# Optimization experiments

Hardware: AMD Instinct MI355X
Metric: run time of the kernel (lower is better)

## Reference

```python
import jax, jax.numpy as jnp
import numpy as np

B, C, D = 512, 100000, 512
MARGIN = 0.5  # ArcFace-style additive angular margin


def setup_inputs() -> dict:
    key = jax.random.key(0)
    k1, k2, k3 = jax.random.split(key, 3)
    embeddings = jax.random.normal(k1, (B, D), dtype=jnp.float32)
    labels = jax.random.randint(k2, (B,), 0, C, dtype=jnp.int32)
    weight = 0.01 * jax.random.normal(k3, (C, D), dtype=jnp.float32)  # torch.normal(0, 0.01, (C, D))
    return {"embeddings": embeddings, "labels": labels, "weight": weight}


def _l2_normalize(x, eps=1e-12):
    return x / jnp.maximum(jnp.linalg.norm(x, axis=-1, keepdims=True), eps)


def reference(embeddings, labels, weight):
    cos_m = jnp.cos(MARGIN)
    sin_m = jnp.sin(MARGIN)

    e = _l2_normalize(embeddings)          # (B, D)
    w = _l2_normalize(weight)              # (C, D)
    logits = jnp.clip(jnp.einsum('bd,cd->bc', e, w), -1.0, 1.0)  # (B, C) cosines

    bsz, ncls = logits.shape
    rows = jnp.arange(bsz)
    cos_t = logits[rows, labels]                                   # (B,) cos(theta_y)
    sin_t = jnp.sqrt(jnp.clip(1.0 - cos_t * cos_t, 0.0, None))     # sin(theta_y)
    cos_tm = cos_t * cos_m - sin_t * sin_m                         # cos(theta_y + m)
    sin_tm = sin_t * cos_m + cos_t * sin_m                         # sin(theta_y + m)

    # non-target class indices per row, ascending, skipping the target: (B, C-1)
    base = jnp.arange(ncls - 1)[None, :]
    nt_idx = base + (base >= labels[:, None]).astype(base.dtype)

    # margin_softmax: logits2 = cos(theta_j) - cos(theta_y + m) over non-target j
    nt_logits = jnp.take_along_axis(logits, nt_idx, axis=1)       # (B, C-1)
    logits2 = nt_logits - cos_tm[:, None]

    # no_grad block: weight_m is unit-norm point at angle theta_y+m from e,
    # so ||w_j - w_m||^2 = 2 - 2 <w_j, w_m>  (avoids materializing (B, C, D)).
    w_y = w[labels]                                                # (B, D)
    w_m = (-sin_m * e + sin_tm[:, None] * w_y) / sin_t[:, None]    # (B, D), unit norm
    sim = jnp.einsum('bd,cd->bc', w_m, w)                          # (B, C)
    nt_sim = jnp.take_along_axis(sim, nt_idx, axis=1)              # (B, C-1)
    diff_weight_norm = jax.lax.stop_gradient(
        jnp.sqrt(jnp.clip(2.0 - 2.0 * nt_sim, 0.0, None)))         # (B, C-1)

    e_logits = jnp.sum(jnp.exp(logits2 / diff_weight_norm), axis=1)  # (B,)
    return jnp.mean(jnp.log1p(e_logits))
```

## Files before the change

### kernel.cpp

```cpp
#include <hip/hip_runtime.h>
#include <hip/hip_fp8.h>
#include <math.h>

#define B_SZ 512
#define C_SZ 100000
#define D_SZ 512

#define BM 128
#define BN 128
#define BK 64
#define NTILES 782
#define MT 8
#define NBLK (NTILES * MT)
#define KSTEPS 8
#define DEPTH 2

typedef __attribute__((ext_vector_type(4))) float f32x4;
typedef __attribute__((ext_vector_type(16))) float f32x16;
typedef __attribute__((ext_vector_type(4))) int i32x4;
typedef __attribute__((ext_vector_type(8))) int i32x8;

#define UNITY_SCALE 0x7F7F7F7F

__device__ __forceinline__ void gload_lds16(const void* gptr, void* lptr) {
  __builtin_amdgcn_global_load_lds(
      (const __attribute__((address_space(1))) void*)gptr,
      (__attribute__((address_space(3))) void*)lptr,
      16, 0, 0);
}

__device__ __forceinline__ unsigned char f2fp8(float x) {
  __hip_fp8_e4m3 h(x);
  return (unsigned char)h.__x;
}
__device__ __forceinline__ float fp82f(unsigned int u) {
  __hip_fp8_e4m3 h;
  h.__x = (unsigned char)u;
  return (float)h;
}
__device__ __forceinline__ unsigned int pack4f8(float a, float b, float c, float d) {
  return (unsigned int)f2fp8(a) | ((unsigned int)f2fp8(b) << 8) |
         ((unsigned int)f2fp8(c) << 16) | ((unsigned int)f2fp8(d) << 24);
}

__device__ __forceinline__ i32x8 ld_frag(const unsigned char* base, int frag, int l) {
  i32x4 lo = *(const i32x4*)(base + frag * 2048 + l * 16);
  i32x4 hg = *(const i32x4*)(base + frag * 2048 + 1024 + l * 16);
  return __builtin_shufflevector(lo, hg, 0, 1, 2, 3, 4, 5, 6, 7);
}

__global__ __launch_bounds__(256) void k_norm_w(const float* __restrict__ w,
                                                unsigned char* __restrict__ w8) {
  const int row = blockIdx.x * 4 + (threadIdx.x >> 6);
  const int lane = threadIdx.x & 63;
  const float4* wr = (const float4*)(w + (size_t)row * D_SZ);
  float4 v0 = wr[lane];
  float4 v1 = wr[64 + lane];
  float ss = v0.x*v0.x + v0.y*v0.y + v0.z*v0.z + v0.w*v0.w
           + v1.x*v1.x + v1.y*v1.y + v1.z*v1.z + v1.w*v1.w;
  #pragma unroll
  for (int o = 32; o; o >>= 1) ss += __shfl_xor(ss, o, 64);
  const float rn = __builtin_amdgcn_rsqf(fmaxf(ss, 1e-24f));
  unsigned int* out = (unsigned int*)(w8 + (size_t)row * D_SZ);
  out[lane] = pack4f8(v0.x * rn, v0.y * rn, v0.z * rn, v0.w * rn);
  out[64 + lane] = pack4f8(v1.x * rn, v1.y * rn, v1.z * rn, v1.w * rn);
}

__global__ __launch_bounds__(64) void k_prep(const float* __restrict__ e,
                                             const int* __restrict__ labels,
                                             const unsigned char* __restrict__ w8,
                                             unsigned char* __restrict__ A8,
                                             float4* __restrict__ params) {
  const int b = blockIdx.x;
  const int lane = threadIdx.x;
  const float4* er = (const float4*)(e + (size_t)b * D_SZ);
  float4 v0 = er[lane], v1 = er[64 + lane];
  float ss = v0.x*v0.x + v0.y*v0.y + v0.z*v0.z + v0.w*v0.w
           + v1.x*v1.x + v1.y*v1.y + v1.z*v1.z + v1.w*v1.w;
  #pragma unroll
  for (int o = 32; o; o >>= 1) ss += __shfl_xor(ss, o, 64);
  const float rn = __builtin_amdgcn_rsqf(fmaxf(ss, 1e-24f));
  v0.x *= rn; v0.y *= rn; v0.z *= rn; v0.w *= rn;
  v1.x *= rn; v1.y *= rn; v1.z *= rn; v1.w *= rn;

  unsigned int* arow_e = (unsigned int*)(A8 + (size_t)(2 * b) * D_SZ);
  arow_e[lane] = pack4f8(v0.x, v0.y, v0.z, v0.w);
  arow_e[64 + lane] = pack4f8(v1.x, v1.y, v1.z, v1.w);

  const int lab = labels[b];
  const unsigned int* wr = (const unsigned int*)(w8 + (size_t)lab * D_SZ);
  unsigned int w0 = wr[lane], w1 = wr[64 + lane];
  unsigned int* arow_w = (unsigned int*)(A8 + (size_t)(2 * b + 1) * D_SZ);
  arow_w[lane] = w0;
  arow_w[64 + lane] = w1;

  float d = v0.x * fp82f(w0 & 255) + v0.y * fp82f((w0 >> 8) & 255)
          + v0.z * fp82f((w0 >> 16) & 255) + v0.w * fp82f(w0 >> 24)
          + v1.x * fp82f(w1 & 255) + v1.y * fp82f((w1 >> 8) & 255)
          + v1.z * fp82f((w1 >> 16) & 255) + v1.w * fp82f(w1 >> 24);
  #pragma unroll
  for (int o = 32; o; o >>= 1) d += __shfl_xor(d, o, 64);

  if (lane == 0) {
    const float cos_m = 0.877582561890372716f;
    const float sin_m = 0.479425538604203000f;
    float cos_t = fminf(fmaxf(d, -1.0f), 1.0f);
    float sin_t = sqrtf(fmaxf(1.0f - cos_t * cos_t, 0.0f));
    float cos_tm = cos_t * cos_m - sin_t * sin_m;
    float sin_tm = sin_t * cos_m + cos_t * sin_m;
    float inv_st = 1.0f / fmaxf(sin_t, 1e-20f);
    params[b] = make_float4(cos_tm, sin_m * inv_st, sin_tm * inv_st, 0.0f);
  }
}

__device__ __forceinline__ float termf(float de, float dwy, float4 p, bool kill) {
  float c = fminf(fmaxf(de, -1.0f), 1.0f);
  float s = p.z * dwy - p.y * de;
  float x = fmaxf(fmaf(-2.0f, s, 2.0f), 1e-20f);
  float t = (c - p.x) * __builtin_amdgcn_rsqf(x);
  float r = __expf(t);
  return kill ? 0.0f : r;
}

__global__ __launch_bounds__(512, 8) void k_gemm(const unsigned char* __restrict__ A8,
                                                 const unsigned char* __restrict__ W8,
                                                 const float4* __restrict__ params,
                                                 const int* __restrict__ labels,
                                                 float* __restrict__ part) {
  __shared__ __align__(32) unsigned char At[DEPTH][BM * BK];
  __shared__ __align__(32) unsigned char Bt[DEPTH][BN * BK];
  __shared__ float ered[64];
  __shared__ float4 pl[64];
  __shared__ int ll[64];

  const int bid = blockIdx.x;
  const int p = (bid & 7) * (NBLK / 8) + (bid >> 3);
  const int nt = p >> 3, mt = p & 7;
  const int t = threadIdx.x;
  const int w = t >> 6, l = t & 63;
  const int m0 = mt * BM;
  const int n0 = nt * BN;
  const int b0 = mt * 64;

  if (t < 64) {
    ered[t] = 0.0f;
    pl[t] = params[b0 + t];
    ll[t] = labels[b0 + t];
  }

  const int kpart = ((t >> 5) & 1) * 32 + ((t >> 6) & 1) * 16;
  const int aoffs = (m0 + (t >> 7) * 32 + (t & 31)) * D_SZ + kpart;
  int brow_s = n0 + (t >> 7) * 32 + (t & 31);
  if (brow_s >= C_SZ) brow_s = C_SZ - 1;
  const int boffs = brow_s * D_SZ + kpart;

  f32x16 accA = {}, accB = {};
  const int fA = w & 3;
  const int fB0 = (w >> 2) * 2;
  const int hi = l >> 5;

#define STAGE(d, ts)                                                        \
  do {                                                                      \
    const int k0_ = (ts) * BK;                                              \
    gload_lds16(A8 + aoffs + k0_, (void*)(At[d] + t * 16));                 \
    gload_lds16(W8 + (size_t)(boffs + k0_), (void*)(Bt[d] + t * 16));       \
  } while (0)

  STAGE(0, 0);
  STAGE(1, 1);
  asm volatile("s_waitcnt vmcnt(2) lgkmcnt(0)" ::: "memory");
  __builtin_amdgcn_s_barrier();

  #pragma unroll
  for (int s = 0; s < KSTEPS; ++s) {
    const int d = s & 1;
    i32x8 av = ld_frag(At[d], fA, l);
    i32x8 bv = ld_frag(Bt[d], fB0, l);
    __builtin_amdgcn_s_setprio(1);
    accA = __builtin_amdgcn_mfma_scale_f32_32x32x64_f8f6f4(
        av, bv, accA, 0, 0, 0, UNITY_SCALE, 0, UNITY_SCALE);
    bv = ld_frag(Bt[d], fB0 + 1, l);
    accB = __builtin_amdgcn_mfma_scale_f32_32x32x64_f8f6f4(
        av, bv, accB, 0, 0, 0, UNITY_SCALE, 0, UNITY_SCALE);
    __builtin_amdgcn_s_setprio(0);
    if (s < KSTEPS - 1) {
      asm volatile("s_waitcnt vmcnt(0)" ::: "memory");
      __builtin_amdgcn_s_barrier();
      if (s + 2 < KSTEPS)
        STAGE(d, s + 2);
    }
  }
#undef STAGE

  #pragma unroll
  for (int rp = 0; rp < 8; ++rp) {
    const int r = 2 * rp;
    const int lb = fA * 16 + (rp & 1) + 4 * (rp >> 1) + 2 * hi;
    float4 pp = pl[lb];
    int lab = ll[lb];
    int j0 = n0 + fB0 * 32 + (l & 31);
    int j1 = j0 + 32;
    float s = termf(accA[r], accA[r + 1], pp, (j0 >= C_SZ) || (j0 == lab))
            + termf(accB[r], accB[r + 1], pp, (j1 >= C_SZ) || (j1 == lab));
    #pragma unroll
    for (int o = 1; o < 32; o <<= 1) s += __shfl_xor(s, o, 64);
    if ((l & 31) == 0) atomicAdd(&ered[lb], s);
  }
  __syncthreads();
  if (t < 64) part[(size_t)(b0 + t) * NTILES + nt] = ered[t];
}

__global__ __launch_bounds__(256) void k_rowsum(const float* __restrict__ part,
                                                float* __restrict__ rowsum) {
  const int b = blockIdx.x;
  float s = 0.0f;
  for (int i = threadIdx.x; i < NTILES; i += 256) s += part[(size_t)b * NTILES + i];
  #pragma unroll
  for (int o = 32; o; o >>= 1) s += __shfl_xor(s, o, 64);
  __shared__ float red[4];
  if ((threadIdx.x & 63) == 0) red[threadIdx.x >> 6] = s;
  __syncthreads();
  if (threadIdx.x == 0)
    rowsum[b] = log1pf(red[0] + red[1] + red[2] + red[3]);
}

__global__ __launch_bounds__(512) void k_final(const float* __restrict__ rowsum,
                                               float* __restrict__ out) {
  const int b = threadIdx.x;
  float v = rowsum[b];
  __shared__ float red[512];
  red[b] = v;
  __syncthreads();
  #pragma unroll
  for (int o = 256; o; o >>= 1) {
    if (b < o) red[b] += red[b + o];
    __syncthreads();
  }
  if (b == 0) out[0] = red[0] / (float)B_SZ;
}

extern "C" void kernel_launch(void* const* d_in, const int* in_sizes, int n_in,
                              void* d_out, int out_size, void* d_ws, size_t ws_size,
                              hipStream_t stream) {
  const float* emb = (const float*)d_in[0];
  const int* labels = (const int*)d_in[1];
  const float* w = (const float*)d_in[2];

  char* ws = (char*)d_ws;
  unsigned char* w8 = (unsigned char*)ws;
  size_t off = (size_t)C_SZ * D_SZ;
  unsigned char* A8 = (unsigned char*)(ws + off);
  off += (size_t)2 * B_SZ * D_SZ;
  float4* params = (float4*)(ws + off);
  off += (size_t)B_SZ * 16;
  float* part = (float*)(ws + off);
  off += (size_t)B_SZ * NTILES * 4;
  float* rowsum = (float*)(ws + off);
  off += (size_t)B_SZ * 4;

  k_norm_w<<<dim3(C_SZ / 4), dim3(256), 0, stream>>>(w, w8);
  k_prep<<<dim3(B_SZ), dim3(64), 0, stream>>>(emb, labels, w8, A8, params);
  k_gemm<<<dim3(NBLK), dim3(512), 0, stream>>>(A8, w8, params, labels, part);
  k_rowsum<<<dim3(B_SZ), dim3(256), 0, stream>>>(part, rowsum);
  k_final<<<dim3(1), dim3(512), 0, stream>>>(rowsum, (float*)d_out);
}
```

Measured before the change: 146.6 us.

## Double GEMM block M-tile to 256 with 2x2 MFMA accumulators per wave

Raises the block M tile from 128 to 256 rows, so each wave computes a 2x2 grid of 32x32 MFMA outputs instead of 1x2, and halves the number of blocks along M. Each loaded W tile is reused across twice as many rows, cutting global and LDS traffic per MFMA. In exchange it uses more LDS and accumulator registers per block, lowers the occupancy hint from 8 to 4, and spreads the epilogue over more rows per block.

```diff
diff --git a/kernel.cpp b/kernel.cpp
--- a/kernel.cpp
+++ b/kernel.cpp
@@ -6,11 +6,11 @@
 #define C_SZ 100000
 #define D_SZ 512
 
-#define BM 128
+#define BM 256
 #define BN 128
 #define BK 64
 #define NTILES 782
-#define MT 8
+#define MT 4
 #define NBLK (NTILES * MT)
 #define KSTEPS 8
 #define DEPTH 2
@@ -122,66 +122,75 @@
   return kill ? 0.0f : r;
 }
 
-__global__ __launch_bounds__(512, 8) void k_gemm(const unsigned char* __restrict__ A8,
+__global__ __launch_bounds__(512, 4) void k_gemm(const unsigned char* __restrict__ A8,
                                                  const unsigned char* __restrict__ W8,
                                                  const float4* __restrict__ params,
                                                  const int* __restrict__ labels,
                                                  float* __restrict__ part) {
   __shared__ __align__(32) unsigned char At[DEPTH][BM * BK];
   __shared__ __align__(32) unsigned char Bt[DEPTH][BN * BK];
-  __shared__ float ered[64];
-  __shared__ float4 pl[64];
-  __shared__ int ll[64];
+  __shared__ float ered[128];
+  __shared__ float4 pl[128];
+  __shared__ int ll[128];
 
   const int bid = blockIdx.x;
   const int p = (bid & 7) * (NBLK / 8) + (bid >> 3);
-  const int nt = p >> 3, mt = p & 7;
+  const int nt = p >> 2, mt = p & 3;
   const int t = threadIdx.x;
   const int w = t >> 6, l = t & 63;
   const int m0 = mt * BM;
   const int n0 = nt * BN;
-  const int b0 = mt * 64;
-
-  if (t < 64) {
+  const int b0 = mt * 128;
+
+  if (t < 128) {
     ered[t] = 0.0f;
     pl[t] = params[b0 + t];
     ll[t] = labels[b0 + t];
   }
 
   const int kpart = ((t >> 5) & 1) * 32 + ((t >> 6) & 1) * 16;
-  const int aoffs = (m0 + (t >> 7) * 32 + (t & 31)) * D_SZ + kpart;
+  const int aoffs0 = (m0 + (t >> 7) * 32 + (t & 31)) * D_SZ + kpart;
+  const int aoffs1 = aoffs0 + 128 * D_SZ;
   int brow_s = n0 + (t >> 7) * 32 + (t & 31);
   if (brow_s >= C_SZ) brow_s = C_SZ - 1;
   const int boffs = brow_s * D_SZ + kpart;
 
-  f32x16 accA = {}, accB = {};
-  const int fA = w & 3;
+  f32x16 acc00 = {}, acc01 = {}, acc10 = {}, acc11 = {};
+  const int fA0 = (w & 3) * 2;
   const int fB0 = (w >> 2) * 2;
   const int hi = l >> 5;
 
 #define STAGE(d, ts)                                                        \
   do {                                                                      \
     const int k0_ = (ts) * BK;                                              \
-    gload_lds16(A8 + aoffs + k0_, (void*)(At[d] + t * 16));                 \
+    gload_lds16(A8 + aoffs0 + k0_, (void*)(At[d] + t * 16));                \
+    gload_lds16(A8 + aoffs1 + k0_, (void*)(At[d] + 8192 + t * 16));         \
     gload_lds16(W8 + (size_t)(boffs + k0_), (void*)(Bt[d] + t * 16));       \
   } while (0)
 
   STAGE(0, 0);
   STAGE(1, 1);
-  asm volatile("s_waitcnt vmcnt(2) lgkmcnt(0)" ::: "memory");
+  asm volatile("s_waitcnt vmcnt(3) lgkmcnt(0)" ::: "memory");
   __builtin_amdgcn_s_barrier();
 
   #pragma unroll
   for (int s = 0; s < KSTEPS; ++s) {
     const int d = s & 1;
-    i32x8 av = ld_frag(At[d], fA, l);
+    i32x8 av0 = ld_frag(At[d], fA0, l);
+    i32x8 av1 = ld_frag(At[d], fA0 + 1, l);
     i32x8 bv = ld_frag(Bt[d], fB0, l);
     __builtin_amdgcn_s_setprio(1);
-    accA = __builtin_amdgcn_mfma_scale_f32_32x32x64_f8f6f4(
-        av, bv, accA, 0, 0, 0, UNITY_SCALE, 0, UNITY_SCALE);
+    acc00 = __builtin_amdgcn_mfma_scale_f32_32x32x64_f8f6f4(
+        av0, bv, acc00, 0, 0, 0, UNITY_SCALE, 0, UNITY_SCALE);
+    acc10 = __builtin_amdgcn_mfma_scale_f32_32x32x64_f8f6f4(
+        av1, bv, acc10, 0, 0, 0, UNITY_SCALE, 0, UNITY_SCALE);
+    __builtin_amdgcn_s_setprio(0);
     bv = ld_frag(Bt[d], fB0 + 1, l);
-    accB = __builtin_amdgcn_mfma_scale_f32_32x32x64_f8f6f4(
-        av, bv, accB, 0, 0, 0, UNITY_SCALE, 0, UNITY_SCALE);
+    __builtin_amdgcn_s_setprio(1);
+    acc01 = __builtin_amdgcn_mfma_scale_f32_32x32x64_f8f6f4(
+        av0, bv, acc01, 0, 0, 0, UNITY_SCALE, 0, UNITY_SCALE);
+    acc11 = __builtin_amdgcn_mfma_scale_f32_32x32x64_f8f6f4(
+        av1, bv, acc11, 0, 0, 0, UNITY_SCALE, 0, UNITY_SCALE);
     __builtin_amdgcn_s_setprio(0);
     if (s < KSTEPS - 1) {
       asm volatile("s_waitcnt vmcnt(0)" ::: "memory");
@@ -195,19 +204,32 @@
   #pragma unroll
   for (int rp = 0; rp < 8; ++rp) {
     const int r = 2 * rp;
-    const int lb = fA * 16 + (rp & 1) + 4 * (rp >> 1) + 2 * hi;
-    float4 pp = pl[lb];
-    int lab = ll[lb];
-    int j0 = n0 + fB0 * 32 + (l & 31);
-    int j1 = j0 + 32;
-    float s = termf(accA[r], accA[r + 1], pp, (j0 >= C_SZ) || (j0 == lab))
-            + termf(accB[r], accB[r + 1], pp, (j1 >= C_SZ) || (j1 == lab));
-    #pragma unroll
-    for (int o = 1; o < 32; o <<= 1) s += __shfl_xor(s, o, 64);
-    if ((l & 31) == 0) atomicAdd(&ered[lb], s);
+    const int rowk = (rp & 1) + 4 * (rp >> 1) + 2 * hi;
+    const int j0 = n0 + fB0 * 32 + (l & 31);
+    const int j1 = j0 + 32;
+    {
+      const int lb = fA0 * 16 + rowk;
+      float4 pp = pl[lb];
+      int lab = ll[lb];
+      float s = termf(acc00[r], acc00[r + 1], pp, (j0 >= C_SZ) || (j0 == lab))
+              + termf(acc01[r], acc01[r + 1], pp, (j1 >= C_SZ) || (j1 == lab));
+      #pragma unroll
+      for (int o = 1; o < 32; o <<= 1) s += __shfl_xor(s, o, 64);
+      if ((l & 31) == 0) atomicAdd(&ered[lb], s);
+    }
+    {
+      const int lb = (fA0 + 1) * 16 + rowk;
+      float4 pp = pl[lb];
+      int lab = ll[lb];
+      float s = termf(acc10[r], acc10[r + 1], pp, (j0 >= C_SZ) || (j0 == lab))
+              + termf(acc11[r], acc11[r + 1], pp, (j1 >= C_SZ) || (j1 == lab));
+      #pragma unroll
+      for (int o = 1; o < 32; o <<= 1) s += __shfl_xor(s, o, 64);
+      if ((l & 31) == 0) atomicAdd(&ered[lb], s);
+    }
   }
   __syncthreads();
-  if (t < 64) part[(size_t)(b0 + t) * NTILES + nt] = ered[t];
+  if (t < 128) part[(size_t)(b0 + t) * NTILES + nt] = ered[t];
 }
 
 __global__ __launch_bounds__(256) void k_rowsum(const float* __restrict__ part,
```

Result: slower. 151.6 us (+3.4%).

## Pre-swizzle A operand into MFMA fragment layout and load directly from global

Applied to the files above, without the earlier changes.

k_prep now writes the interleaved embedding/target-weight A matrix straight into the per-lane MFMA fragment order. The GEMM kernel then reads the A fragments with two 16-byte global loads per k-step instead of staging them through LDS, so the A shared-memory buffers and their async copies go away. This halves the LDS traffic and footprint per block, which may help occupancy. The cost is that A loads now sit in the MFMA dependency chain without double-buffered prefetch, and the cache reuse of the small A matrix decides whether that latency is hidden.

```diff
diff --git a/kernel.cpp b/kernel.cpp
--- a/kernel.cpp
+++ b/kernel.cpp
@@ -69,7 +69,7 @@
 __global__ __launch_bounds__(64) void k_prep(const float* __restrict__ e,
                                              const int* __restrict__ labels,
                                              const unsigned char* __restrict__ w8,
-                                             unsigned char* __restrict__ A8,
+                                             unsigned char* __restrict__ A8f,
                                              float4* __restrict__ params) {
   const int b = blockIdx.x;
   const int lane = threadIdx.x;
@@ -83,16 +83,27 @@
   v0.x *= rn; v0.y *= rn; v0.z *= rn; v0.w *= rn;
   v1.x *= rn; v1.y *= rn; v1.z *= rn; v1.w *= rn;
 
-  unsigned int* arow_e = (unsigned int*)(A8 + (size_t)(2 * b) * D_SZ);
-  arow_e[lane] = pack4f8(v0.x, v0.y, v0.z, v0.w);
-  arow_e[64 + lane] = pack4f8(v1.x, v1.y, v1.z, v1.w);
+  const unsigned int ue0 = pack4f8(v0.x, v0.y, v0.z, v0.w);
+  const unsigned int ue1 = pack4f8(v1.x, v1.y, v1.z, v1.w);
 
   const int lab = labels[b];
   const unsigned int* wr = (const unsigned int*)(w8 + (size_t)lab * D_SZ);
-  unsigned int w0 = wr[lane], w1 = wr[64 + lane];
-  unsigned int* arow_w = (unsigned int*)(A8 + (size_t)(2 * b + 1) * D_SZ);
-  arow_w[lane] = w0;
-  arow_w[64 + lane] = w1;
+  const unsigned int w0 = wr[lane], w1 = wr[64 + lane];
+
+  const int re = 2 * b;
+  const int frag = re >> 5;
+  const int rife = re & 31;
+  const int wk = (4 * lane) & 63;
+  const int ks = lane >> 4;
+  const int sbits = (((wk >> 5) & 1) << 5) | (((wk >> 4) & 1) << 6);
+  const int byteo = wk & 15;
+  unsigned char* fb = A8f + (size_t)frag * 16384;
+  unsigned char* pe = fb + (rife | sbits) * 16 + byteo;
+  unsigned char* pw = fb + ((rife + 1) | sbits) * 16 + byteo;
+  *(unsigned int*)(pe + ks * 2048) = ue0;
+  *(unsigned int*)(pe + (ks + 4) * 2048) = ue1;
+  *(unsigned int*)(pw + ks * 2048) = w0;
+  *(unsigned int*)(pw + (ks + 4) * 2048) = w1;
 
   float d = v0.x * fp82f(w0 & 255) + v0.y * fp82f((w0 >> 8) & 255)
           + v0.z * fp82f((w0 >> 16) & 255) + v0.w * fp82f(w0 >> 24)
@@ -122,12 +133,11 @@
   return kill ? 0.0f : r;
 }
 
-__global__ __launch_bounds__(512, 8) void k_gemm(const unsigned char* __restrict__ A8,
+__global__ __launch_bounds__(512, 8) void k_gemm(const unsigned char* __restrict__ A8f,
                                                  const unsigned char* __restrict__ W8,
                                                  const float4* __restrict__ params,
                                                  const int* __restrict__ labels,
                                                  float* __restrict__ part) {
-  __shared__ __align__(32) unsigned char At[DEPTH][BM * BK];
   __shared__ __align__(32) unsigned char Bt[DEPTH][BN * BK];
   __shared__ float ered[64];
   __shared__ float4 pl[64];
@@ -138,7 +148,6 @@
   const int nt = p >> 3, mt = p & 7;
   const int t = threadIdx.x;
   const int w = t >> 6, l = t & 63;
-  const int m0 = mt * BM;
   const int n0 = nt * BN;
   const int b0 = mt * 64;
 
@@ -149,10 +158,12 @@
   }
 
   const int kpart = ((t >> 5) & 1) * 32 + ((t >> 6) & 1) * 16;
-  const int aoffs = (m0 + (t >> 7) * 32 + (t & 31)) * D_SZ + kpart;
   int brow_s = n0 + (t >> 7) * 32 + (t & 31);
   if (brow_s >= C_SZ) brow_s = C_SZ - 1;
   const int boffs = brow_s * D_SZ + kpart;
+
+  const unsigned char* afb =
+      A8f + (size_t)(mt * 4 + (w & 3)) * 16384 + l * 16;
 
   f32x16 accA = {}, accB = {};
   const int fA = w & 3;
@@ -160,21 +171,19 @@
   const int hi = l >> 5;
 
 #define STAGE(d, ts)                                                        \
-  do {                                                                      \
-    const int k0_ = (ts) * BK;                                              \
-    gload_lds16(A8 + aoffs + k0_, (void*)(At[d] + t * 16));                 \
-    gload_lds16(W8 + (size_t)(boffs + k0_), (void*)(Bt[d] + t * 16));       \
-  } while (0)
+  gload_lds16(W8 + (size_t)(boffs + (ts) * BK), (void*)(Bt[d] + t * 16))
 
   STAGE(0, 0);
   STAGE(1, 1);
-  asm volatile("s_waitcnt vmcnt(2) lgkmcnt(0)" ::: "memory");
+  asm volatile("s_waitcnt vmcnt(1) lgkmcnt(0)" ::: "memory");
   __builtin_amdgcn_s_barrier();
 
   #pragma unroll
   for (int s = 0; s < KSTEPS; ++s) {
     const int d = s & 1;
-    i32x8 av = ld_frag(At[d], fA, l);
+    i32x4 alo = *(const i32x4*)(afb + s * 2048);
+    i32x4 ahi = *(const i32x4*)(afb + s * 2048 + 1024);
+    i32x8 av = __builtin_shufflevector(alo, ahi, 0, 1, 2, 3, 4, 5, 6, 7);
     i32x8 bv = ld_frag(Bt[d], fB0, l);
     __builtin_amdgcn_s_setprio(1);
     accA = __builtin_amdgcn_mfma_scale_f32_32x32x64_f8f6f4(
@@ -249,7 +258,7 @@
   char* ws = (char*)d_ws;
   unsigned char* w8 = (unsigned char*)ws;
   size_t off = (size_t)C_SZ * D_SZ;
-  unsigned char* A8 = (unsigned char*)(ws + off);
+  unsigned char* A8f = (unsigned char*)(ws + off);
   off += (size_t)2 * B_SZ * D_SZ;
   float4* params = (float4*)(ws + off);
   off += (size_t)B_SZ * 16;
@@ -259,8 +268,8 @@
   off += (size_t)B_SZ * 4;
 
   k_norm_w<<<dim3(C_SZ / 4), dim3(256), 0, stream>>>(w, w8);
-  k_prep<<<dim3(B_SZ), dim3(64), 0, stream>>>(emb, labels, w8, A8, params);
-  k_gemm<<<dim3(NBLK), dim3(512), 0, stream>>>(A8, w8, params, labels, part);
+  k_prep<<<dim3(B_SZ), dim3(64), 0, stream>>>(emb, labels, w8, A8f, params);
+  k_gemm<<<dim3(NBLK), dim3(512), 0, stream>>>(A8f, w8, params, labels, part);
   k_rowsum<<<dim3(B_SZ), dim3(256), 0, stream>>>(part, rowsum);
   k_final<<<dim3(1), dim3(512), 0, stream>>>(rowsum, (float*)d_out);
 }
```

Result: slower. 377.0 us (+157.2%).
